# Optimization experiments

Measured on AMD Instinct MI355X. Metric: run time of the kernel, lower is better.

The kernel has to match this reference:

```python
import jax, jax.numpy as jnp
import numpy as np

N = 10000
E = 160000
DIMS = [512, 512, 512, 256]  # in -> hidden -> hidden -> out (num_layers=3)
EPS = 1e-12  # F.normalize default eps


def _sage_layer(x, edge_index, Wl, b, Wr):
    # PyG SAGEConv (mean aggr, normalize=True):
    # out = lin_l(mean_{j in N(i)} x_j) + lin_r(x_i), then L2-normalize rows.
    src = edge_index[0]
    dst = edge_index[1]
    msg = x[src]  # [E, d] gather of source-node features
    agg = jax.ops.segment_sum(msg, dst, num_segments=N)  # [N, d]
    cnt = jax.ops.segment_sum(jnp.ones((E,), x.dtype), dst, num_segments=N)
    mean = agg / jnp.maximum(cnt, 1.0)[:, None]
    out = mean @ Wl.T + b + x @ Wr.T
    norm = jnp.sqrt(jnp.sum(out * out, axis=-1, keepdims=True))
    return out / jnp.maximum(norm, EPS)


def setup_inputs() -> dict:
    key = jax.random.key(0)
    ks = jax.random.split(key, 2 + 3 * len(DIMS))
    x = jax.random.normal(ks[0], (N, DIMS[0]), dtype=jnp.float32)
    edge_index = jax.random.randint(ks[1], (2, E), 0, N, dtype=jnp.int64)
    inp = {"x": x, "edge_index": edge_index}
    k = 2
    for i in range(len(DIMS) - 1):
        din, dout = DIMS[i], DIMS[i + 1]
        s = 1.0 / np.sqrt(din)
        inp[f"Wl{i}"] = jax.random.uniform(ks[k], (dout, din), jnp.float32, -s, s); k += 1
        inp[f"b{i}"] = jax.random.uniform(ks[k], (dout,), jnp.float32, -s, s); k += 1
        inp[f"Wr{i}"] = jax.random.uniform(ks[k], (dout, din), jnp.float32, -s, s); k += 1
    return inp


def reference(x, edge_index, Wl0, b0, Wr0, Wl1, b1, Wr1, Wl2, b2, Wr2):
    params = [(Wl0, b0, Wr0), (Wl1, b1, Wr1), (Wl2, b2, Wr2)]
    for Wl, b, Wr in params:
        x = _sage_layer(x, edge_index, Wl, b, Wr)
        x = jax.nn.relu(x)
        # F.dropout(training=False) is identity at inference
    return x
```

## Files before the change

kernel.cpp:

```cpp
#include <hip/hip_runtime.h>

#define NN 10000

typedef __attribute__((ext_vector_type(8))) short short8;
typedef __attribute__((ext_vector_type(4))) float f32x4;

__device__ __forceinline__ ushort f2b(float f) {
    union { float f; uint32_t u; } v; v.f = f;
    uint32_t u = v.u;
    return (ushort)((u + 0x7fffu + ((u >> 16) & 1u)) >> 16);
}
__device__ __forceinline__ uint packbf(float a, float b) {
    return (uint)f2b(a) | ((uint)f2b(b) << 16);
}
__device__ __forceinline__ float blo(uint u) {
    union { uint u; float f; } v; v.u = u << 16; return v.f;
}
__device__ __forceinline__ float bhi(uint u) {
    union { uint u; float f; } v; v.u = u & 0xffff0000u; return v.f;
}

__global__ __launch_bounds__(256) void zero_int(int* __restrict__ p, int n) {
    int i = blockIdx.x * 256 + threadIdx.x;
    if (i < n) p[i] = 0;
}

__global__ __launch_bounds__(256) void count_dst(const int* __restrict__ dst,
                                                 int* __restrict__ counts, int E) {
    int i = blockIdx.x * 256 + threadIdx.x;
    if (i < E) atomicAdd(&counts[dst[i]], 1);
}

__global__ __launch_bounds__(1024) void scan_build(const int* __restrict__ counts,
                                                   int* __restrict__ offsets,
                                                   int* __restrict__ cursor,
                                                   float* __restrict__ inv_cnt, int n) {
    __shared__ int part[1024];
    int tid = threadIdx.x;
    int per = (n + 1023) / 1024;
    int base = tid * per;
    int s = 0;
    for (int i = 0; i < per; i++) { int idx = base + i; if (idx < n) s += counts[idx]; }
    part[tid] = s;
    __syncthreads();
    for (int off = 1; off < 1024; off <<= 1) {
        int v = (tid >= off) ? part[tid - off] : 0;
        __syncthreads();
        part[tid] += v;
        __syncthreads();
    }
    int run = (tid > 0) ? part[tid - 1] : 0;
    for (int i = 0; i < per; i++) {
        int idx = base + i;
        if (idx < n) {
            int c = counts[idx];
            offsets[idx] = run;
            cursor[idx]  = run;
            inv_cnt[idx] = 1.0f / fmaxf((float)c, 1.0f);
            run += c;
        }
    }
}

__global__ __launch_bounds__(256) void scatter_edges(const int* __restrict__ src,
                                                     const int* __restrict__ dst,
                                                     int* __restrict__ cursor,
                                                     int* __restrict__ sorted_src, int E) {
    int i = blockIdx.x * 256 + threadIdx.x;
    if (i < E) {
        int p = atomicAdd(&cursor[dst[i]], 1);
        sorted_src[p] = src[i];
    }
}

__global__ __launch_bounds__(256) void cvt_x2(const float* __restrict__ in,
                                              ushort* __restrict__ out, int n4) {
    int i = blockIdx.x * 256 + threadIdx.x;
    if (i >= n4) return;
    int idx = i * 4;
    float4 v = *(const float4*)(in + idx);
    uint2 p;
    p.x = packbf(v.x, v.y);
    p.y = packbf(v.z, v.w);
    *(uint2*)(out + idx) = p;
}

__global__ __launch_bounds__(256) void cvt_w2(const float* __restrict__ Wl,
                                              const float* __restrict__ Wr,
                                              ushort* __restrict__ out,
                                              int dout, int n4) {
    int i = blockIdx.x * 256 + threadIdx.x;
    if (i >= n4) return;
    int idx = i * 4;
    int row = idx >> 9;
    int col = idx & 511;
    const float* src = (row < dout) ? (Wl + (size_t)row * 512 + col)
                                    : (Wr + (size_t)(row - dout) * 512 + col);
    float4 v = *(const float4*)src;
    uint2 p;
    p.x = packbf(v.x, v.y);
    p.y = packbf(v.z, v.w);
    *(uint2*)(out + idx) = p;
}

__global__ __launch_bounds__(256) void gemm_split(const ushort* __restrict__ A,
                                                  const ushort* __restrict__ B,
                                                  ushort* __restrict__ G,
                                                  float* __restrict__ R,
                                                  int M, int dout) {
    __shared__ ushort Asl[128 * 32];
    __shared__ ushort Bsl[128 * 32];
    const int tid  = threadIdx.x;
    const int w    = tid >> 6;
    const int lane = tid & 63;
    const int bm = blockIdx.y * 128, bn = blockIdx.x * 128;
    const int wm = (w & 1) * 64, wn = (w >> 1) * 64;
    const int row16 = lane & 15, q = lane >> 4;

    f32x4 acc[4][4];
#pragma unroll
    for (int i = 0; i < 4; i++)
#pragma unroll
        for (int j = 0; j < 4; j++) acc[i][j] = (f32x4){0.f, 0.f, 0.f, 0.f};

    const int sc_r = lane >> 2;
    const int sc_s = lane & 3;
    const int koff = sc_s ^ ((sc_r >> 1) & 3);
    const int swz  = (row16 >> 1) & 3;

    for (int k0 = 0; k0 < 512; k0 += 32) {
#pragma unroll
        for (int c = 0; c < 2; c++) {
            int chunk = w * 2 + c;
            int rloc  = chunk * 16 + sc_r;
            int growA = bm + rloc; growA = growA < M ? growA : M - 1;
            const ushort* gpA = A + (size_t)growA * 512 + k0 + koff * 8;
            __builtin_amdgcn_global_load_lds(
                (const __attribute__((address_space(1))) uint32_t*)gpA,
                (__attribute__((address_space(3))) uint32_t*)&Asl[chunk * 512],
                16, 0, 0);
            const ushort* gpB = B + (size_t)(bn + rloc) * 512 + k0 + koff * 8;
            __builtin_amdgcn_global_load_lds(
                (const __attribute__((address_space(1))) uint32_t*)gpB,
                (__attribute__((address_space(3))) uint32_t*)&Bsl[chunk * 512],
                16, 0, 0);
        }
        __syncthreads();

        short8 af[4], bfr[4];
        int s = q ^ swz;
#pragma unroll
        for (int i = 0; i < 4; i++) {
            int r = wm + i * 16 + row16;
            af[i] = *(const short8*)&Asl[r * 32 + s * 8];
        }
#pragma unroll
        for (int j = 0; j < 4; j++) {
            int rn = wn + j * 16 + row16;
            bfr[j] = *(const short8*)&Bsl[rn * 32 + s * 8];
        }
#pragma unroll
        for (int i = 0; i < 4; i++)
#pragma unroll
            for (int j = 0; j < 4; j++)
                acc[i][j] = __builtin_amdgcn_mfma_f32_16x16x32_bf16(
                    af[i], bfr[j], acc[i][j], 0, 0, 0);
        __syncthreads();
    }

    const bool isR = (bn >= dout);
#pragma unroll
    for (int i = 0; i < 4; i++) {
#pragma unroll
        for (int r2 = 0; r2 < 4; r2++) {
            int row = bm + wm + i * 16 + q * 4 + r2;
            if (row < M) {
                if (isR) {
                    float* Rp = R + (size_t)row * dout + (bn - dout) + wn + row16;
#pragma unroll
                    for (int j = 0; j < 4; j++)
                        Rp[j * 16] = acc[i][j][r2];
                } else {
                    ushort* Gp = G + (size_t)row * dout + bn + wn + row16;
#pragma unroll
                    for (int j = 0; j < 4; j++)
                        Gp[j * 16] = f2b(acc[i][j][r2]);
                }
            }
        }
    }
}

template <int DOUT, bool FINAL>
__global__ __launch_bounds__(256) void aggfin(const ushort* __restrict__ G,
                                              const float* __restrict__ R,
                                              const float* __restrict__ bias,
                                              const int* __restrict__ offsets,
                                              const int* __restrict__ counts,
                                              const int* __restrict__ sorted_src,
                                              const float* __restrict__ inv_cnt,
                                              ushort* __restrict__ xnext,
                                              float* __restrict__ outf, int n) {
    constexpr int PL = DOUT / 64;
    int wave = threadIdx.x >> 6;
    int lane = threadIdx.x & 63;
    int node = blockIdx.x * 4 + wave;
    if (node >= n) return;
    int start = offsets[node];
    int cnt   = counts[node];
    float inv = inv_cnt[node];

    float acc[PL];
#pragma unroll
    for (int k = 0; k < PL; k++) acc[k] = 0.f;

    if constexpr (DOUT == 512) {
        const uint* gp = (const uint*)G + lane * 4;
#define ACC8(v) do { \
        acc[0] += blo(v.x); acc[1] += bhi(v.x); \
        acc[2] += blo(v.y); acc[3] += bhi(v.y); \
        acc[4] += blo(v.z); acc[5] += bhi(v.z); \
        acc[6] += blo(v.w); acc[7] += bhi(v.w); } while (0)
        int e = 0;
        for (; e + 8 <= cnt; e += 8) {
            uint4 vv[8];
#pragma unroll
            for (int u = 0; u < 8; u++) {
                int s0 = sorted_src[start + e + u];
                vv[u] = *(const uint4*)(gp + (size_t)s0 * 256);
            }
#pragma unroll
            for (int u = 0; u < 8; u++) ACC8(vv[u]);
        }
        for (; e < cnt; e++) {
            int s0 = sorted_src[start + e];
            uint4 v0 = *(const uint4*)(gp + (size_t)s0 * 256);
            ACC8(v0);
        }
#undef ACC8
    } else {
        const uint* gp = (const uint*)G + lane * 2;
#define ACC4(v) do { \
        acc[0] += blo(v.x); acc[1] += bhi(v.x); \
        acc[2] += blo(v.y); acc[3] += bhi(v.y); } while (0)
        int e = 0;
        for (; e + 8 <= cnt; e += 8) {
            uint2 vv[8];
#pragma unroll
            for (int u = 0; u < 8; u++) {
                int s0 = sorted_src[start + e + u];
                vv[u] = *(const uint2*)(gp + (size_t)s0 * 128);
            }
#pragma unroll
            for (int u = 0; u < 8; u++) ACC4(vv[u]);
        }
        for (; e < cnt; e++) {
            int s0 = sorted_src[start + e];
            uint2 v0 = *(const uint2*)(gp + (size_t)s0 * 128);
            ACC4(v0);
        }
#undef ACC4
    }

    float v[PL];
    const float* Rp = R + (size_t)node * DOUT + lane * PL;
    const float* Bp = bias + lane * PL;
#pragma unroll
    for (int k = 0; k < PL; k += 4) {
        float4 r4 = *(const float4*)(Rp + k);
        float4 b4 = *(const float4*)(Bp + k);
        v[k + 0] = acc[k + 0] * inv + r4.x + b4.x;
        v[k + 1] = acc[k + 1] * inv + r4.y + b4.y;
        v[k + 2] = acc[k + 2] * inv + r4.z + b4.z;
        v[k + 3] = acc[k + 3] * inv + r4.w + b4.w;
    }
    float ss = 0.f;
#pragma unroll
    for (int k = 0; k < PL; k++) ss += v[k] * v[k];
#pragma unroll
    for (int m = 32; m >= 1; m >>= 1) ss += __shfl_xor(ss, m, 64);
    float scale = 1.0f / fmaxf(sqrtf(ss), 1e-12f);

    if constexpr (FINAL) {
        float* Op = outf + (size_t)node * DOUT + lane * PL;
#pragma unroll
        for (int k = 0; k < PL; k += 4) {
            float4 o;
            o.x = fmaxf(v[k + 0] * scale, 0.f);
            o.y = fmaxf(v[k + 1] * scale, 0.f);
            o.z = fmaxf(v[k + 2] * scale, 0.f);
            o.w = fmaxf(v[k + 3] * scale, 0.f);
            *(float4*)(Op + k) = o;
        }
    } else {
        uint4 o;
        float r0 = fmaxf(v[0] * scale, 0.f), r1 = fmaxf(v[1] * scale, 0.f);
        float r2 = fmaxf(v[2] * scale, 0.f), r3 = fmaxf(v[3] * scale, 0.f);
        float r4 = fmaxf(v[4] * scale, 0.f), r5 = fmaxf(v[5] * scale, 0.f);
        float r6 = fmaxf(v[6] * scale, 0.f), r7 = fmaxf(v[7] * scale, 0.f);
        o.x = packbf(r0, r1); o.y = packbf(r2, r3);
        o.z = packbf(r4, r5); o.w = packbf(r6, r7);
        *(uint4*)(xnext + (size_t)node * 512 + lane * 8) = o;
    }
}

extern "C" void kernel_launch(void* const* d_in, const int* in_sizes, int n_in,
                              void* d_out, int out_size, void* d_ws, size_t ws_size,
                              hipStream_t stream) {
    const float* x    = (const float*)d_in[0];
    const int*   edge = (const int*)d_in[1];
    const float* Wl0  = (const float*)d_in[2];
    const float* b0   = (const float*)d_in[3];
    const float* Wr0  = (const float*)d_in[4];
    const float* Wl1  = (const float*)d_in[5];
    const float* b1   = (const float*)d_in[6];
    const float* Wr1  = (const float*)d_in[7];
    const float* Wl2  = (const float*)d_in[8];
    const float* b2   = (const float*)d_in[9];
    const float* Wr2  = (const float*)d_in[10];

    const int E = in_sizes[1] / 2;

    char* ws = (char*)d_ws;
    int*    counts  = (int*)(ws + 0);
    int*    offsets = (int*)(ws + 40960);
    int*    cursor  = (int*)(ws + 81920);
    float*  invc    = (float*)(ws + 122880);
    int*    sorted  = (int*)(ws + 163840);
    ushort* Wc0     = (ushort*)(ws + 819200);
    ushort* Wc1     = (ushort*)(ws + 1867776);
    ushort* Wc2     = (ushort*)(ws + 2916352);
    ushort* xbuf    = (ushort*)(ws + 3440640);
    ushort* Gbuf    = (ushort*)(ws + 13680640);
    float*  Rbuf    = (float*)(ws + 23920640);

    zero_int<<<(NN + 255) / 256, 256, 0, stream>>>(counts, NN);
    count_dst<<<(E + 255) / 256, 256, 0, stream>>>(edge + E, counts, E);
    scan_build<<<1, 1024, 0, stream>>>(counts, offsets, cursor, invc, NN);
    scatter_edges<<<(E + 255) / 256, 256, 0, stream>>>(edge, edge + E, cursor, sorted, E);

    cvt_x2<<<(NN * 512 / 4 + 255) / 256, 256, 0, stream>>>(x, xbuf, NN * 512 / 4);
    cvt_w2<<<(1024 * 512 / 4 + 255) / 256, 256, 0, stream>>>(Wl0, Wr0, Wc0, 512, 1024 * 512 / 4);
    cvt_w2<<<(1024 * 512 / 4 + 255) / 256, 256, 0, stream>>>(Wl1, Wr1, Wc1, 512, 1024 * 512 / 4);
    cvt_w2<<<(512 * 512 / 4 + 255) / 256, 256, 0, stream>>>(Wl2, Wr2, Wc2, 256, 512 * 512 / 4);

    const int gyM = (NN + 127) / 128;
    const int gb  = (NN + 3) / 4;

    gemm_split<<<dim3(8, gyM), 256, 0, stream>>>(xbuf, Wc0, Gbuf, Rbuf, NN, 512);
    aggfin<512, false><<<gb, 256, 0, stream>>>(Gbuf, Rbuf, b0, offsets, counts,
                                               sorted, invc, xbuf, nullptr, NN);
    gemm_split<<<dim3(8, gyM), 256, 0, stream>>>(xbuf, Wc1, Gbuf, Rbuf, NN, 512);
    aggfin<512, false><<<gb, 256, 0, stream>>>(Gbuf, Rbuf, b1, offsets, counts,
                                               sorted, invc, xbuf, nullptr, NN);
    gemm_split<<<dim3(4, gyM), 256, 0, stream>>>(xbuf, Wc2, Gbuf, Rbuf, NN, 256);
    aggfin<256, true><<<gb, 256, 0, stream>>>(Gbuf, Rbuf, b2, offsets, counts,
                                              sorted, invc, nullptr, (float*)d_out, NN);
}
```

Before: 275.1 us.

## Double-buffer GEMM LDS tiles, swizzle blocks across XCDs, merge conversion kernels

The GEMM now keeps two LDS buffers and issues the next k-tile's global-to-LDS loads before computing on the current one, so load latency can overlap with MFMA work, at the cost of twice the shared memory. Workgroup IDs are remapped so that consecutive tiles land on the same XCD, which is meant to improve L2 reuse. The four fp32-to-bf16 conversion launches are merged into one kernel with hardcoded range boundaries, removing launch overhead.

```diff
diff --git a/kernel.cpp b/kernel.cpp
--- a/kernel.cpp
+++ b/kernel.cpp
@@ -73,34 +73,50 @@
     }
 }
 
-__global__ __launch_bounds__(256) void cvt_x2(const float* __restrict__ in,
-                                              ushort* __restrict__ out, int n4) {
+__global__ __launch_bounds__(256) void cvt_all(const float* __restrict__ x,
+                                               const float* __restrict__ Wl0,
+                                               const float* __restrict__ Wr0,
+                                               const float* __restrict__ Wl1,
+                                               const float* __restrict__ Wr1,
+                                               const float* __restrict__ Wl2,
+                                               const float* __restrict__ Wr2,
+                                               ushort* __restrict__ xbuf,
+                                               ushort* __restrict__ Wc0,
+                                               ushort* __restrict__ Wc1,
+                                               ushort* __restrict__ Wc2) {
     int i = blockIdx.x * 256 + threadIdx.x;
-    if (i >= n4) return;
-    int idx = i * 4;
-    float4 v = *(const float4*)(in + idx);
-    uint2 p;
-    p.x = packbf(v.x, v.y);
-    p.y = packbf(v.z, v.w);
-    *(uint2*)(out + idx) = p;
-}
-
-__global__ __launch_bounds__(256) void cvt_w2(const float* __restrict__ Wl,
-                                              const float* __restrict__ Wr,
-                                              ushort* __restrict__ out,
-                                              int dout, int n4) {
-    int i = blockIdx.x * 256 + threadIdx.x;
-    if (i >= n4) return;
-    int idx = i * 4;
-    int row = idx >> 9;
-    int col = idx & 511;
-    const float* src = (row < dout) ? (Wl + (size_t)row * 512 + col)
-                                    : (Wr + (size_t)(row - dout) * 512 + col);
+    const float* src;
+    ushort* dst;
+    if (i < 1280000) {
+        int idx = i * 4;
+        src = x + idx;
+        dst = xbuf + idx;
+    } else if (i < 1411072) {
+        int j = (i - 1280000) * 4;
+        int row = j >> 9, col = j & 511;
+        src = (row < 512) ? (Wl0 + (size_t)row * 512 + col)
+                          : (Wr0 + (size_t)(row - 512) * 512 + col);
+        dst = Wc0 + j;
+    } else if (i < 1542144) {
+        int j = (i - 1411072) * 4;
+        int row = j >> 9, col = j & 511;
+        src = (row < 512) ? (Wl1 + (size_t)row * 512 + col)
+                          : (Wr1 + (size_t)(row - 512) * 512 + col);
+        dst = Wc1 + j;
+    } else if (i < 1607680) {
+        int j = (i - 1542144) * 4;
+        int row = j >> 9, col = j & 511;
+        src = (row < 256) ? (Wl2 + (size_t)row * 512 + col)
+                          : (Wr2 + (size_t)(row - 256) * 512 + col);
+        dst = Wc2 + j;
+    } else {
+        return;
+    }
     float4 v = *(const float4*)src;
     uint2 p;
     p.x = packbf(v.x, v.y);
     p.y = packbf(v.z, v.w);
-    *(uint2*)(out + idx) = p;
+    *(uint2*)dst = p;
 }
 
 __global__ __launch_bounds__(256) void gemm_split(const ushort* __restrict__ A,
@@ -108,12 +124,21 @@
                                                   ushort* __restrict__ G,
                                                   float* __restrict__ R,
                                                   int M, int dout) {
-    __shared__ ushort Asl[128 * 32];
-    __shared__ ushort Bsl[128 * 32];
+    __shared__ ushort Asl[2][128 * 32];
+    __shared__ ushort Bsl[2][128 * 32];
     const int tid  = threadIdx.x;
     const int w    = tid >> 6;
     const int lane = tid & 63;
-    const int bm = blockIdx.y * 128, bn = blockIdx.x * 128;
+
+    const int nbx = gridDim.x, nby = gridDim.y;
+    const int nwg = nbx * nby;
+    const int id  = blockIdx.y * nbx + blockIdx.x;
+    const int qq  = nwg >> 3, rr = nwg & 7;
+    const int xcd = id & 7, blk = id >> 3;
+    const int swzid = (xcd < rr ? xcd * (qq + 1) : rr * (qq + 1) + (xcd - rr) * qq) + blk;
+    const int bx = swzid % nbx, by = swzid / nbx;
+
+    const int bm = by * 128, bn = bx * 128;
     const int wm = (w & 1) * 64, wn = (w >> 1) * 64;
     const int row16 = lane & 15, q = lane >> 4;
 
@@ -128,7 +153,7 @@
     const int koff = sc_s ^ ((sc_r >> 1) & 3);
     const int swz  = (row16 >> 1) & 3;
 
-    for (int k0 = 0; k0 < 512; k0 += 32) {
+    auto stage = [&](int buf, int k0) {
 #pragma unroll
         for (int c = 0; c < 2; c++) {
             int chunk = w * 2 + c;
@@ -137,27 +162,35 @@
             const ushort* gpA = A + (size_t)growA * 512 + k0 + koff * 8;
             __builtin_amdgcn_global_load_lds(
                 (const __attribute__((address_space(1))) uint32_t*)gpA,
-                (__attribute__((address_space(3))) uint32_t*)&Asl[chunk * 512],
+                (__attribute__((address_space(3))) uint32_t*)&Asl[buf][chunk * 512],
                 16, 0, 0);
             const ushort* gpB = B + (size_t)(bn + rloc) * 512 + k0 + koff * 8;
             __builtin_amdgcn_global_load_lds(
                 (const __attribute__((address_space(1))) uint32_t*)gpB,
-                (__attribute__((address_space(3))) uint32_t*)&Bsl[chunk * 512],
+                (__attribute__((address_space(3))) uint32_t*)&Bsl[buf][chunk * 512],
                 16, 0, 0);
         }
-        __syncthreads();
+    };
+
+    const int NT = 512 / 32;
+    stage(0, 0);
+    __syncthreads();
+    int cur = 0;
+
+    for (int t = 0; t < NT; ++t) {
+        if (t + 1 < NT) stage(cur ^ 1, (t + 1) * 32);
 
         short8 af[4], bfr[4];
         int s = q ^ swz;
 #pragma unroll
         for (int i = 0; i < 4; i++) {
             int r = wm + i * 16 + row16;
-            af[i] = *(const short8*)&Asl[r * 32 + s * 8];
+            af[i] = *(const short8*)&Asl[cur][r * 32 + s * 8];
         }
 #pragma unroll
         for (int j = 0; j < 4; j++) {
             int rn = wn + j * 16 + row16;
-            bfr[j] = *(const short8*)&Bsl[rn * 32 + s * 8];
+            bfr[j] = *(const short8*)&Bsl[cur][rn * 32 + s * 8];
         }
 #pragma unroll
         for (int i = 0; i < 4; i++)
@@ -165,7 +198,9 @@
             for (int j = 0; j < 4; j++)
                 acc[i][j] = __builtin_amdgcn_mfma_f32_16x16x32_bf16(
                     af[i], bfr[j], acc[i][j], 0, 0, 0);
+
         __syncthreads();
+        cur ^= 1;
     }
 
     const bool isR = (bn >= dout);
@@ -339,10 +374,8 @@
     scan_build<<<1, 1024, 0, stream>>>(counts, offsets, cursor, invc, NN);
     scatter_edges<<<(E + 255) / 256, 256, 0, stream>>>(edge, edge + E, cursor, sorted, E);
 
-    cvt_x2<<<(NN * 512 / 4 + 255) / 256, 256, 0, stream>>>(x, xbuf, NN * 512 / 4);
-    cvt_w2<<<(1024 * 512 / 4 + 255) / 256, 256, 0, stream>>>(Wl0, Wr0, Wc0, 512, 1024 * 512 / 4);
-    cvt_w2<<<(1024 * 512 / 4 + 255) / 256, 256, 0, stream>>>(Wl1, Wr1, Wc1, 512, 1024 * 512 / 4);
-    cvt_w2<<<(512 * 512 / 4 + 255) / 256, 256, 0, stream>>>(Wl2, Wr2, Wc2, 256, 512 * 512 / 4);
+    cvt_all<<<(1607680 + 255) / 256, 256, 0, stream>>>(x, Wl0, Wr0, Wl1, Wr1, Wl2, Wr2,
+                                                       xbuf, Wc0, Wc1, Wc2);
 
     const int gyM = (NN + 127) / 128;
     const int gb  = (NN + 3) / 4;
```

Measured after the change: 251.6 us. 1.09x faster.
